# Kernel optimization log

Hardware: AMD Instinct MI355X
Metric: run time of the kernel (lower is better)

## Reference

```python
import jax, jax.numpy as jnp
import numpy as np

B, L, C, H = 4, 2048, 1024, 16
D = C // H  # head_dim = 64


def setup_inputs() -> dict:
    key = jax.random.key(0)
    ks = jax.random.split(key, 7)
    x = jax.random.normal(ks[0], (B, L, C), dtype=jnp.float32)
    Wqkv = jax.random.normal(ks[1], (C, 3 * C), dtype=jnp.float32) * 0.02
    bqkv = jnp.zeros((3 * C,), dtype=jnp.float32)
    q_gamma = jnp.ones((H, D), dtype=jnp.float32)
    k_gamma = jnp.ones((H, D), dtype=jnp.float32)
    Wout = jax.random.normal(ks[2], (C, C), dtype=jnp.float32) * 0.02
    bout = jnp.zeros((C,), dtype=jnp.float32)
    return {"x": x, "Wqkv": Wqkv, "bqkv": bqkv, "q_gamma": q_gamma,
            "k_gamma": k_gamma, "Wout": Wout, "bout": bout}


def _mh_rms_norm(t, gamma):
    # F.normalize(x.float(), dim=-1) * gamma * sqrt(dim), cast back to input dtype
    tf = t.astype(jnp.float32)
    n = jnp.sqrt(jnp.sum(tf * tf, axis=-1, keepdims=True))
    normed = tf / jnp.maximum(n, 1e-12)
    return (normed * gamma * jnp.sqrt(jnp.float32(t.shape[-1]))).astype(t.dtype)


def reference(x, Wqkv, bqkv, q_gamma, k_gamma, Wout, bout):
    b, l, c = x.shape
    qkv = (x @ Wqkv + bqkv).reshape(b, l, 3, H, D)
    q, k, v = qkv[:, :, 0], qkv[:, :, 1], qkv[:, :, 2]  # [B, L, H, D]
    q = _mh_rms_norm(q, q_gamma)
    k = _mh_rms_norm(k, k_gamma)
    # scaled dot-product attention in BLHD layout
    scale = 1.0 / jnp.sqrt(jnp.float32(D))
    scores = jnp.einsum('blhd,bmhd->bhlm', q, k) * scale  # [B, H, L, L]
    probs = jax.nn.softmax(scores, axis=-1)
    h = jnp.einsum('bhlm,bmhd->blhd', probs, v)  # [B, L, H, D]
    h = h.reshape(b, l, c)
    return h @ Wout + bout
```

## Files before the change

kernel.cpp:

```cpp
#include <hip/hip_runtime.h>
#include <hip/hip_bf16.h>
#include <cstdint>
#include <cstddef>

#define B_ 4
#define L_ 2048
#define C_ 1024
#define H_ 16
#define D_ 64

typedef __bf16    bf16x2 __attribute__((ext_vector_type(2)));
typedef __bf16    bf16x4 __attribute__((ext_vector_type(4)));
typedef __bf16    bf16x8 __attribute__((ext_vector_type(8)));
typedef _Float16  f16x4  __attribute__((ext_vector_type(4)));
typedef _Float16  f16x8  __attribute__((ext_vector_type(8)));
typedef float     f32x4  __attribute__((ext_vector_type(4)));
typedef float     f32x16 __attribute__((ext_vector_type(16)));
typedef uint32_t  u32x4  __attribute__((ext_vector_type(4)));

typedef const __attribute__((address_space(1))) uint32_t* gas_ptr;
typedef __attribute__((address_space(3))) uint32_t* las_ptr;
__device__ __forceinline__ void gl_lds16(const void* g, void* l) {
    __builtin_amdgcn_global_load_lds((gas_ptr)(uintptr_t)g,
                                     (las_ptr)(uintptr_t)l, 16, 0, 0);
}

__device__ __forceinline__ uint32_t cvtpk_bf16(float lo, float hi) {
    uint32_t r;
    asm("v_cvt_pk_bf16_f32 %0, %1, %2" : "=v"(r) : "v"(lo), "v"(hi));
    return r;
}
__device__ __forceinline__ void plswap(uint32_t& a, uint32_t& b) {
    asm("v_permlane32_swap_b32 %0, %1" : "+v"(a), "+v"(b));
}

__global__ __launch_bounds__(256) void prep_kernel(
    const float* __restrict__ x, _Float16* __restrict__ x16,
    const float* __restrict__ Wqkv, _Float16* __restrict__ Wq16,
    const float* __restrict__ Wout, _Float16* __restrict__ Wo16)
{
    __shared__ float tile[64][65];
    int bid = blockIdx.x;
    const int tid = threadIdx.x;

    if (bid < 8192) {
        int i = (bid * 256 + tid) * 4;
        float4 v = *(const float4*)&x[i];
        f16x4 o = {(_Float16)v.x, (_Float16)v.y, (_Float16)v.z, (_Float16)v.w};
        *(f16x4*)&x16[i] = o;
        return;
    }
    bid -= 8192;
    const float* W; _Float16* Wt; int N, tx, ty;
    if (bid < 768) { W = Wqkv; Wt = Wq16; N = 3072; tx = bid % 48; ty = bid / 48; }
    else { bid -= 768; W = Wout; Wt = Wo16; N = 1024; tx = bid % 16; ty = bid / 16; }
    const int K = 1024;
    const int k0 = ty * 64, n0 = tx * 64;
    for (int i = tid; i < 1024; i += 256) {
        int r = i >> 4, c4 = (i & 15) * 4;
        float4 v = *(const float4*)&W[(size_t)(k0 + r) * N + n0 + c4];
        tile[r][c4 + 0] = v.x; tile[r][c4 + 1] = v.y;
        tile[r][c4 + 2] = v.z; tile[r][c4 + 3] = v.w;
    }
    __syncthreads();
    for (int i = tid; i < 1024; i += 256) {
        int n = i >> 4, k4 = (i & 15) * 4;
        f16x4 o = {(_Float16)tile[k4 + 0][n], (_Float16)tile[k4 + 1][n],
                   (_Float16)tile[k4 + 2][n], (_Float16)tile[k4 + 3][n]};
        *(f16x4*)&Wt[(size_t)(n0 + n) * K + k0 + k4] = o;
    }
}

template <int MODE>
__global__ __launch_bounds__(256) void gemm_f16_bt_kernel(
    const _Float16* __restrict__ A, const _Float16* __restrict__ Bt,
    const float* __restrict__ bias, void* __restrict__ Cout,
    __bf16* __restrict__ vTout, const float* __restrict__ q_gamma,
    const float* __restrict__ k_gamma, int M, int N, int K)
{
    __shared__ __align__(16) char smraw[16384];
    _Float16* Ash = (_Float16*)smraw;
    _Float16* Bsh = Ash + 128 * 32;

    const int tid  = threadIdx.x;
    const int lane = tid & 63;
    const int wv   = tid >> 6;
    const int wm   = wv & 1, wn = wv >> 1;
    const int n16  = lane & 15, quad = lane >> 4;
    const int brow = blockIdx.y * 128;
    const int bcol = blockIdx.x * 128;

    const int srow = lane >> 2;
    const int scol = (lane & 3) * 8;
    const _Float16* gA = A  + (size_t)(brow + wv * 32 + srow) * K + scol;
    const _Float16* gB = Bt + (size_t)(bcol + wv * 32 + srow) * K + scol;
    _Float16* lA0 = &Ash[wv * 1024];
    _Float16* lA1 = &Ash[wv * 1024 + 512];
    _Float16* lB0 = &Bsh[wv * 1024];
    _Float16* lB1 = &Bsh[wv * 1024 + 512];

    f32x4 acc[4][4] = {};

    for (int k0 = 0; k0 < K; k0 += 32) {
        gl_lds16(gA + k0,                  lA0);
        gl_lds16(gA + k0 + 16 * (size_t)K, lA1);
        gl_lds16(gB + k0,                  lB0);
        gl_lds16(gB + k0 + 16 * (size_t)K, lB1);
        __syncthreads();

        f16x8 ar[4], br[4];
        #pragma unroll
        for (int t = 0; t < 4; t++) {
            ar[t] = *(const f16x8*)&Ash[(wm * 64 + t * 16 + n16) * 32 + quad * 8];
            br[t] = *(const f16x8*)&Bsh[(wn * 64 + t * 16 + n16) * 32 + quad * 8];
        }
        #pragma unroll
        for (int i = 0; i < 4; i++)
            #pragma unroll
            for (int j = 0; j < 4; j++)
                acc[i][j] = __builtin_amdgcn_mfma_f32_16x16x32_f16(
                    ar[i], br[j], acc[i][j], 0, 0, 0);
        __syncthreads();
    }

    if (MODE == 0) {
        #pragma unroll
        for (int j = 0; j < 4; j++) {
            const int col = bcol + wn * 64 + j * 16 + n16;
            const float bv = bias[col];
            #pragma unroll
            for (int i = 0; i < 4; i++) {
                const int row0 = brow + wm * 64 + i * 16 + quad * 4;
                #pragma unroll
                for (int r = 0; r < 4; r++)
                    ((float*)Cout)[(size_t)(row0 + r) * N + col] = acc[i][j][r] + bv;
            }
        }
        return;
    }

    const int region = bcol >> 10;
    float bj[4];
    #pragma unroll
    for (int j = 0; j < 4; j++) bj[j] = bias[bcol + wn * 64 + j * 16 + n16];

    if (region < 2) {
        const float* gamma = (region == 0) ? q_gamma : k_gamma;
        const float scl = (region == 0) ? 1.44269504f : 8.0f;
        const int cb = (bcol & 1023) + wn * 64 + n16;
        float gj[4];
        #pragma unroll
        for (int j = 0; j < 4; j++) gj[j] = gamma[cb + j * 16];

        #pragma unroll
        for (int i = 0; i < 4; i++) {
            #pragma unroll
            for (int r = 0; r < 4; r++) {
                float v0 = acc[i][0][r] + bj[0];
                float v1 = acc[i][1][r] + bj[1];
                float v2 = acc[i][2][r] + bj[2];
                float v3 = acc[i][3][r] + bj[3];
                float ss = v0 * v0 + v1 * v1 + v2 * v2 + v3 * v3;
                ss += __shfl_xor(ss, 1, 64);
                ss += __shfl_xor(ss, 2, 64);
                ss += __shfl_xor(ss, 4, 64);
                ss += __shfl_xor(ss, 8, 64);
                const float sc = scl / fmaxf(sqrtf(ss), 1e-12f);
                const int row = brow + wm * 64 + i * 16 + quad * 4 + r;
                __bf16* op = (__bf16*)Cout + (size_t)row * 3072 + bcol + wn * 64 + n16;
                op[ 0] = (__bf16)(v0 * gj[0] * sc);
                op[16] = (__bf16)(v1 * gj[1] * sc);
                op[32] = (__bf16)(v2 * gj[2] * sc);
                op[48] = (__bf16)(v3 * gj[3] * sc);
            }
        }
    } else {
        __bf16* LTb = (__bf16*)smraw;
        const int d    = tid >> 1;
        const int head = ((bcol - 2048) >> 6) + (d >> 6);
        const size_t vb0 = (((size_t)((brow >> 11) * 16 + head)) * 64 + (d & 63)) * 2048
                           + (brow & 2047);
        #pragma unroll
        for (int p = 0; p < 4; p++) {
            if (wm == (p >> 1)) {
                #pragma unroll
                for (int ii = 0; ii < 2; ii++) {
                    const int i = (p & 1) * 2 + ii;
                    #pragma unroll
                    for (int j = 0; j < 4; j++) {
                        const int col  = wn * 64 + j * 16 + n16;
                        const int rowb = ii * 16 + quad * 4;
                        bf16x4 t4 = {(__bf16)(acc[i][j][0] + bj[j]),
                                     (__bf16)(acc[i][j][1] + bj[j]),
                                     (__bf16)(acc[i][j][2] + bj[j]),
                                     (__bf16)(acc[i][j][3] + bj[j])};
                        *(bf16x4*)&LTb[col * 40 + rowb] = t4;
                    }
                }
            }
            __syncthreads();
            #pragma unroll
            for (int s = 0; s < 2; s++) {
                const int chunk = (tid & 1) * 2 + s;
                *(bf16x8*)&vTout[vb0 + p * 32 + chunk * 8] =
                    *(const bf16x8*)&LTb[d * 40 + chunk * 8];
            }
            __syncthreads();
        }
    }
}

__global__ __launch_bounds__(256, 4) void attn_mfma_kernel(
    const __bf16* __restrict__ qkv, const __bf16* __restrict__ vT,
    _Float16* __restrict__ h16)
{
    const int tid  = threadIdx.x;
    const int lane = tid & 63;
    const int wv   = tid >> 6;
    const int l31  = lane & 31;
    const int h    = lane >> 5;
    const int x7   = l31 & 7;
    const int qt = blockIdx.x & 15;
    const int hh = (blockIdx.x >> 4) & 15;
    const int bb = blockIdx.x >> 8;
    const int q0 = qt * 128;
    const int bh = bb * 16 + hh;

    __shared__ __align__(16) __bf16 smem[4 * 4096];
    __bf16* Kbuf = smem;
    __bf16* Vbuf = smem + 2 * 4096;

    const __bf16* kbase = &qkv[(size_t)(bb * L_) * 3072 + 1024 + hh * 64];
    const __bf16* vbase = &vT[(size_t)bh * 64 * 2048];

    const int lr = lane >> 3;
    const int lc = (lane & 7) ^ lr;
    const __bf16* kpre = kbase + (size_t)(wv * 8 + lr) * 3072 + lc * 8;
    const __bf16* vpre = vbase + (size_t)(wv * 8 + lr) * 2048 + lc * 8;
    __bf16* kdst = Kbuf + (wv * 8) * 64;
    __bf16* vdst = Vbuf + (wv * 8) * 64;

    #pragma unroll
    for (int t = 0; t < 2; t++) {
        gl_lds16(kpre + (size_t)t * 32 * 3072, kdst + t * 2048);
        gl_lds16(vpre + (size_t)t * 32 * 2048, vdst + t * 2048);
    }

    bf16x8 qf[4];
    const __bf16* qptr = &qkv[(size_t)(bb * L_ + q0 + wv * 32 + l31) * 3072
                              + hh * 64 + h * 8];
    #pragma unroll
    for (int dk = 0; dk < 4; dk++)
        qf[dk] = *(const bf16x8*)&qptr[dk * 16];

    f32x16 acc0 = {}, acc1 = {};
    float l_run = 0.f;

    __syncthreads();

    for (int j0 = 0, cur = 0; j0 < L_; j0 += 64, cur ^= 1) {
        if (j0 + 64 < L_) {
            #pragma unroll
            for (int t = 0; t < 2; t++) {
                gl_lds16(kpre + (size_t)(j0 + 64 + t * 32) * 3072,
                         kdst + (cur ^ 1) * 4096 + t * 2048);
                gl_lds16(vpre + (j0 + 64) + (size_t)t * 32 * 2048,
                         vdst + (cur ^ 1) * 4096 + t * 2048);
            }
        }
        const __bf16* Kc = Kbuf + cur * 4096;
        const __bf16* Vc = Vbuf + cur * 4096;

        f32x16 St0 = {}, St1 = {};
        __builtin_amdgcn_s_setprio(1);
        #pragma unroll
        for (int dk = 0; dk < 4; dk++) {
            const int co = ((2 * dk + h) ^ x7) * 8;
            bf16x8 k0 = *(const bf16x8*)&Kc[l31 * 64 + co];
            bf16x8 k1 = *(const bf16x8*)&Kc[(32 + l31) * 64 + co];
            St0 = __builtin_amdgcn_mfma_f32_32x32x16_bf16(k0, qf[dk], St0, 0, 0, 0);
            St1 = __builtin_amdgcn_mfma_f32_32x32x16_bf16(k1, qf[dk], St1, 0, 0, 0);
        }
        __builtin_amdgcn_s_setprio(0);

        bf16x8 pf[4];
        float ts = 0.f;
        #pragma unroll
        for (int th = 0; th < 2; th++) {
            float e[16];
            #pragma unroll
            for (int r = 0; r < 16; r++) {
                e[r] = __builtin_amdgcn_exp2f(th == 0 ? St0[r] : St1[r]);
                ts += e[r];
            }
            uint32_t a0 = cvtpk_bf16(e[0], e[1]),  a1 = cvtpk_bf16(e[2], e[3]);
            uint32_t b0 = cvtpk_bf16(e[4], e[5]),  b1 = cvtpk_bf16(e[6], e[7]);
            plswap(a0, b0); plswap(a1, b1);
            u32x4 w0; w0.x = a0; w0.y = a1; w0.z = b0; w0.w = b1;
            pf[th * 2 + 0] = __builtin_bit_cast(bf16x8, w0);
            uint32_t c0 = cvtpk_bf16(e[8], e[9]),   c1 = cvtpk_bf16(e[10], e[11]);
            uint32_t d0 = cvtpk_bf16(e[12], e[13]), d1 = cvtpk_bf16(e[14], e[15]);
            plswap(c0, d0); plswap(c1, d1);
            u32x4 w1; w1.x = c0; w1.y = c1; w1.z = d0; w1.w = d1;
            pf[th * 2 + 1] = __builtin_bit_cast(bf16x8, w1);
        }
        l_run += ts;

        __builtin_amdgcn_s_setprio(1);
        #pragma unroll
        for (int kq = 0; kq < 4; kq++) {
            const int co = ((2 * kq + h) ^ x7) * 8;
            bf16x8 v0 = *(const bf16x8*)&Vc[l31 * 64 + co];
            bf16x8 v1 = *(const bf16x8*)&Vc[(32 + l31) * 64 + co];
            acc0 = __builtin_amdgcn_mfma_f32_32x32x16_bf16(v0, pf[kq], acc0, 0, 0, 0);
            acc1 = __builtin_amdgcn_mfma_f32_32x32x16_bf16(v1, pf[kq], acc1, 0, 0, 0);
        }
        __builtin_amdgcn_s_setprio(0);

        __syncthreads();
    }

    l_run += __shfl_xor(l_run, 32, 64);
    const float linv = 1.0f / l_run;

    const size_t orow = (size_t)(bb * L_ + q0 + wv * 32 + l31) * 1024
                        + hh * 64 + h * 4;
    #pragma unroll
    for (int m = 0; m < 4; m++) {
        f16x4 o0 = {(_Float16)(acc0[4 * m + 0] * linv),
                    (_Float16)(acc0[4 * m + 1] * linv),
                    (_Float16)(acc0[4 * m + 2] * linv),
                    (_Float16)(acc0[4 * m + 3] * linv)};
        *(f16x4*)&h16[orow + 8 * m] = o0;
        f16x4 o1 = {(_Float16)(acc1[4 * m + 0] * linv),
                    (_Float16)(acc1[4 * m + 1] * linv),
                    (_Float16)(acc1[4 * m + 2] * linv),
                    (_Float16)(acc1[4 * m + 3] * linv)};
        *(f16x4*)&h16[orow + 32 + 8 * m] = o1;
    }
}

extern "C" void kernel_launch(void* const* d_in, const int* in_sizes, int n_in,
                              void* d_out, int out_size, void* d_ws, size_t ws_size,
                              hipStream_t stream)
{
    const float* x       = (const float*)d_in[0];
    const float* Wqkv    = (const float*)d_in[1];
    const float* bqkv    = (const float*)d_in[2];
    const float* q_gamma = (const float*)d_in[3];
    const float* k_gamma = (const float*)d_in[4];
    const float* Wout    = (const float*)d_in[5];
    const float* bout    = (const float*)d_in[6];
    float* out = (float*)d_out;

    uint8_t* ws = (uint8_t*)d_ws;
    _Float16* x16   = (_Float16*)(ws);
    _Float16* Wq16  = (_Float16*)(ws + (16ull << 20));
    _Float16* Wo16  = (_Float16*)(ws + (22ull << 20));
    __bf16*   qkv16 = (__bf16*)  (ws + (24ull << 20));
    _Float16* h16   = (_Float16*)(ws + (72ull << 20));
    __bf16*   vT    = (__bf16*)  (ws + (88ull << 20));

    prep_kernel<<<8192 + 768 + 256, 256, 0, stream>>>(x, x16, Wqkv, Wq16, Wout, Wo16);

    gemm_f16_bt_kernel<1><<<dim3(3 * C_ / 128, B_ * L_ / 128), 256, 0, stream>>>(
        x16, Wq16, bqkv, qkv16, vT, q_gamma, k_gamma, B_ * L_, 3 * C_, C_);

    attn_mfma_kernel<<<B_ * H_ * (L_ / 128), 256, 0, stream>>>(qkv16, vT, h16);

    gemm_f16_bt_kernel<0><<<dim3(C_ / 128, B_ * L_ / 128), 256, 0, stream>>>(
        h16, Wo16, bout, out, nullptr, nullptr, nullptr, B_ * L_, C_, C_);
}
```

Baseline: 299.5 us.

## Double GEMM k-tile to 64 with XOR-swizzled LDS and narrower out-proj tiles

The GEMM kernel now stages K-tiles of 64 instead of 32, which halves the number of barrier pairs per output tile. An XOR swizzle on the LDS column chunk is applied to both the global-to-LDS loads and the fragment reads to avoid bank conflicts. The output projection (MODE 0) uses 128x64 tiles, doubling its grid to 1024 blocks so more CUs are occupied. LDS use per block grows, and the smaller N tile lowers arithmetic intensity for the out-projection.

Measured after the change: 289.1 us. 1.04x faster.

```diff
diff --git a/kernel.cpp b/kernel.cpp
--- a/kernel.cpp
+++ b/kernel.cpp
@@ -78,9 +78,11 @@
     __bf16* __restrict__ vTout, const float* __restrict__ q_gamma,
     const float* __restrict__ k_gamma, int M, int N, int K)
 {
-    __shared__ __align__(16) char smraw[16384];
+    constexpr int BN = (MODE == 0) ? 64 : 128;
+    constexpr int NJ = BN / 32;
+    __shared__ __align__(16) char smraw[(128 + BN) * 64 * 2];
     _Float16* Ash = (_Float16*)smraw;
-    _Float16* Bsh = Ash + 128 * 32;
+    _Float16* Bsh = Ash + 128 * 64;
 
     const int tid  = threadIdx.x;
     const int lane = tid & 63;
@@ -88,45 +90,53 @@
     const int wm   = wv & 1, wn = wv >> 1;
     const int n16  = lane & 15, quad = lane >> 4;
     const int brow = blockIdx.y * 128;
-    const int bcol = blockIdx.x * 128;
-
-    const int srow = lane >> 2;
-    const int scol = (lane & 3) * 8;
-    const _Float16* gA = A  + (size_t)(brow + wv * 32 + srow) * K + scol;
-    const _Float16* gB = Bt + (size_t)(bcol + wv * 32 + srow) * K + scol;
-    _Float16* lA0 = &Ash[wv * 1024];
-    _Float16* lA1 = &Ash[wv * 1024 + 512];
-    _Float16* lB0 = &Bsh[wv * 1024];
-    _Float16* lB1 = &Bsh[wv * 1024 + 512];
-
-    f32x4 acc[4][4] = {};
-
-    for (int k0 = 0; k0 < K; k0 += 32) {
-        gl_lds16(gA + k0,                  lA0);
-        gl_lds16(gA + k0 + 16 * (size_t)K, lA1);
-        gl_lds16(gB + k0,                  lB0);
-        gl_lds16(gB + k0 + 16 * (size_t)K, lB1);
+    const int bcol = blockIdx.x * BN;
+
+    const int rr = lane >> 3;
+    const int sw = ((lane & 7) ^ rr) * 8;
+    const _Float16* gA = A  + (size_t)(brow + wv * 32 + rr) * K + sw;
+    const _Float16* gB = Bt + (size_t)(bcol + wv * (BN / 4) + rr) * K + sw;
+    _Float16* lA = &Ash[(wv * 32) * 64];
+    _Float16* lB = &Bsh[(wv * (BN / 4)) * 64];
+
+    f32x4 acc[4][NJ] = {};
+
+    for (int k0 = 0; k0 < K; k0 += 64) {
+        #pragma unroll
+        for (int t = 0; t < 4; t++)
+            gl_lds16(gA + k0 + (size_t)t * 8 * K, lA + t * 8 * 64);
+        #pragma unroll
+        for (int t = 0; t < BN / 32; t++)
+            gl_lds16(gB + k0 + (size_t)t * 8 * K, lB + t * 8 * 64);
         __syncthreads();
 
-        f16x8 ar[4], br[4];
-        #pragma unroll
-        for (int t = 0; t < 4; t++) {
-            ar[t] = *(const f16x8*)&Ash[(wm * 64 + t * 16 + n16) * 32 + quad * 8];
-            br[t] = *(const f16x8*)&Bsh[(wn * 64 + t * 16 + n16) * 32 + quad * 8];
-        }
-        #pragma unroll
-        for (int i = 0; i < 4; i++)
-            #pragma unroll
-            for (int j = 0; j < 4; j++)
-                acc[i][j] = __builtin_amdgcn_mfma_f32_16x16x32_f16(
-                    ar[i], br[j], acc[i][j], 0, 0, 0);
+        #pragma unroll
+        for (int h = 0; h < 2; h++) {
+            f16x8 ar[4], br[NJ];
+            #pragma unroll
+            for (int t = 0; t < 4; t++) {
+                const int row = wm * 64 + t * 16 + n16;
+                ar[t] = *(const f16x8*)&Ash[row * 64 + (((h << 2) | quad) ^ (row & 7)) * 8];
+            }
+            #pragma unroll
+            for (int j = 0; j < NJ; j++) {
+                const int row = wn * (BN / 2) + j * 16 + n16;
+                br[j] = *(const f16x8*)&Bsh[row * 64 + (((h << 2) | quad) ^ (row & 7)) * 8];
+            }
+            #pragma unroll
+            for (int i = 0; i < 4; i++)
+                #pragma unroll
+                for (int j = 0; j < NJ; j++)
+                    acc[i][j] = __builtin_amdgcn_mfma_f32_16x16x32_f16(
+                        ar[i], br[j], acc[i][j], 0, 0, 0);
+        }
         __syncthreads();
     }
 
     if (MODE == 0) {
         #pragma unroll
-        for (int j = 0; j < 4; j++) {
-            const int col = bcol + wn * 64 + j * 16 + n16;
+        for (int j = 0; j < NJ; j++) {
+            const int col = bcol + wn * (BN / 2) + j * 16 + n16;
             const float bv = bias[col];
             #pragma unroll
             for (int i = 0; i < 4; i++) {
@@ -368,6 +378,6 @@
 
     attn_mfma_kernel<<<B_ * H_ * (L_ / 128), 256, 0, stream>>>(qkv16, vT, h16);
 
-    gemm_f16_bt_kernel<0><<<dim3(C_ / 128, B_ * L_ / 128), 256, 0, stream>>>(
+    gemm_f16_bt_kernel<0><<<dim3(C_ / 64, B_ * L_ / 128), 256, 0, stream>>>(
         h16, Wo16, bout, out, nullptr, nullptr, nullptr, B_ * L_, C_, C_);
 }
```
